# Kernel tuning notes

Hardware: AMD Instinct MI355X
Metric: run time of the kernel (lower is better)

## Reference

```python
import math
import jax, jax.numpy as jnp
import numpy as np

D_MODEL = 1024
NUM_HEADS = 16
MAX_SEQ_LEN = 2048
THETA = 10000.0


def setup_inputs() -> dict:
    key = jax.random.key(0)
    ks = jax.random.split(key, 5)
    B, S, D = 2, 2048, D_MODEL
    std = math.sqrt(2.0 / (D + D))
    x = jax.random.normal(ks[0], (B, S, D), dtype=jnp.float32)
    wq = jax.random.normal(ks[1], (D, D), dtype=jnp.float32) * std
    wk = jax.random.normal(ks[2], (D, D), dtype=jnp.float32) * std
    wv = jax.random.normal(ks[3], (D, D), dtype=jnp.float32) * std
    wo = jax.random.normal(ks[4], (D, D), dtype=jnp.float32) * std
    return {"x": x, "wq": wq, "wk": wk, "wv": wv, "wo": wo}


def _rope_tables(seq_len: int, d_k: int):
    # angles[i, k] = i / theta^(2k/d_k), k over d_k//2 pairs
    inv_freq = 1.0 / (THETA ** (jnp.arange(0, d_k, 2, dtype=jnp.float32) / d_k))
    angles = jnp.arange(seq_len, dtype=jnp.float32)[:, None] * inv_freq[None, :]  # [S, d_k/2]
    return jnp.cos(angles), jnp.sin(angles)


def _apply_rope(x, cos, sin):
    # x: [..., S, d_k]; cos/sin: [S, d_k/2], broadcast over leading dims
    x_even = x[..., ::2]
    x_odd = x[..., 1::2]
    r_even = x_even * cos - x_odd * sin
    r_odd = x_even * sin + x_odd * cos
    return jnp.stack([r_even, r_odd], axis=-1).reshape(x.shape)


def reference(x, wq, wk, wv, wo):
    B, S, D = x.shape
    H = NUM_HEADS
    dk = D // H

    def split_heads(t):  # [B,S,D] -> [B,H,S,dk]
        return t.reshape(B, S, H, dk).transpose(0, 2, 1, 3)

    Q = split_heads(x @ wq.T)
    K = split_heads(x @ wk.T)
    V = split_heads(x @ wv.T)

    cos, sin = _rope_tables(S, dk)
    Q = _apply_rope(Q, cos, sin)
    K = _apply_rope(K, cos, sin)

    scores = jnp.einsum('bhqd,bhkd->bhqk', Q, K) / jnp.sqrt(jnp.float32(dk))
    mask = jnp.tril(jnp.ones((S, S), dtype=bool))  # causal: q can attend k <= q
    neg_inf = jnp.float32(-jnp.inf)
    scores = jnp.where(mask, scores, neg_inf)
    m = jnp.max(scores, axis=-1, keepdims=True)
    m = jnp.where(jnp.isinf(m), jnp.zeros_like(m), m)
    exp_scores = jnp.exp(scores - m)
    exp_scores = jnp.where(mask, exp_scores, 0.0)
    attn = exp_scores / (jnp.sum(exp_scores, axis=-1, keepdims=True) + 1e-9)
    out = jnp.einsum('bhqk,bhkd->bhqd', attn, V)  # [B,H,S,dk]
    out = out.transpose(0, 2, 1, 3).reshape(B, S, D)
    return out @ wo.T
```

## Files before the change

### kernel.cpp

```cpp
#include <hip/hip_runtime.h>
#include <stdint.h>

typedef unsigned short u16;
typedef unsigned int u32;
typedef __bf16 bf16x8 __attribute__((ext_vector_type(8)));
typedef float f32x4 __attribute__((ext_vector_type(4)));
typedef unsigned short u16x8 __attribute__((ext_vector_type(8)));

#define D_MODEL 1024
#define SEQ 2048
#define NH 16
#define DK 64
#define NROWS 4096

static __device__ __forceinline__ u16 f2bf(float f) {
  u32 u = __float_as_uint(f);
  u = (u + 0x7FFFu + ((u >> 16) & 1u)) >> 16;
  return (u16)u;
}
static __device__ __forceinline__ float bf2f(u16 h) {
  return __uint_as_float(((u32)h) << 16);
}
static __device__ __forceinline__ f32x4 mfma16(bf16x8 a, bf16x8 b, f32x4 c) {
  return __builtin_amdgcn_mfma_f32_16x16x32_bf16(a, b, c, 0, 0, 0);
}
static __device__ __forceinline__ void gload16(const void* g, void* l) {
  __builtin_amdgcn_global_load_lds(
      (const __attribute__((address_space(1))) void*)g,
      (__attribute__((address_space(3))) void*)l, 16, 0, 0);
}

static __device__ __forceinline__ float xor32_max(float x) {
#if __has_builtin(__builtin_amdgcn_permlane32_swap)
  u32 a = __float_as_uint(x), b = a;
  auto pr = __builtin_amdgcn_permlane32_swap(a, b, false, false);
  return fmaxf(__uint_as_float(pr[0]), __uint_as_float(pr[1]));
#else
  return fmaxf(x, __shfl_xor(x, 32));
#endif
}
static __device__ __forceinline__ float xor32_add(float x) {
#if __has_builtin(__builtin_amdgcn_permlane32_swap)
  u32 a = __float_as_uint(x), b = a;
  auto pr = __builtin_amdgcn_permlane32_swap(a, b, false, false);
  return __uint_as_float(pr[0]) + __uint_as_float(pr[1]);
#else
  return x + __shfl_xor(x, 32);
#endif
}

__global__ __launch_bounds__(256) void k_cast(
    const float* __restrict__ x, const float* __restrict__ wq,
    const float* __restrict__ wk, const float* __restrict__ wv,
    const float* __restrict__ wo, u16* __restrict__ xb, u16* __restrict__ wqb,
    u16* __restrict__ wkb, u16* __restrict__ wvb, u16* __restrict__ wob,
    float* __restrict__ ct, float* __restrict__ st) {
  if (blockIdx.x >= 4096) {
    int i = (int)(blockIdx.x - 4096) * 256 + threadIdx.x;
    int s = i >> 5, p = i & 31;
    double ang = (double)s * pow(10000.0, -(double)p / 32.0);
    ct[i] = (float)cos(ang);
    st[i] = (float)sin(ang);
    return;
  }
  size_t e = ((size_t)blockIdx.x * 256 + threadIdx.x) * 8;
  const float* s;
  u16* d;
  size_t off;
  if (e < (size_t)NROWS * D_MODEL) {
    s = x; d = xb; off = e;
  } else {
    size_t r = e - (size_t)NROWS * D_MODEL;
    unsigned wi = (unsigned)(r >> 20);
    off = r & 1048575u;
    s = wi == 0 ? wq : wi == 1 ? wk : wi == 2 ? wv : wo;
    d = wi == 0 ? wqb : wi == 1 ? wkb : wi == 2 ? wvb : wob;
  }
  float4 a = *(const float4*)(s + off);
  float4 b = *(const float4*)(s + off + 4);
  u16x8 o;
  o[0] = f2bf(a.x); o[1] = f2bf(a.y); o[2] = f2bf(a.z); o[3] = f2bf(a.w);
  o[4] = f2bf(b.x); o[5] = f2bf(b.y); o[6] = f2bf(b.z); o[7] = f2bf(b.w);
  *(u16x8*)(d + off) = o;
}

__global__ __launch_bounds__(256, 1) void k_gemm3(
    const u16* __restrict__ A, const u16* __restrict__ B0,
    const u16* __restrict__ B1, const u16* __restrict__ B2,
    u16* __restrict__ Cb) {
  constexpr int K = 1024;
  const int mb = blockIdx.x, nb = blockIdx.y;
  const int tid = threadIdx.x;
  const int lane = tid & 63, w = tid >> 6;
  const int lq = lane & 15, lg = lane >> 4;
  const int wm = w >> 1, wn = w & 1;
  __shared__ __align__(16) u16 As[128 * 64];
  __shared__ __align__(16) u16 Bs[128 * 64];

  const int sel = nb >> 3;
  const u16* Bp = sel == 0 ? B0 : (sel == 1 ? B1 : B2);
  const int nloc = (nb & 7) * 128;
  const char* Ab = (const char*)A + (size_t)mb * 128 * 2048;
  const char* Bb = (const char*)Bp + (size_t)nloc * 2048;

  f32x4 zero4 = {0.f, 0.f, 0.f, 0.f};
  f32x4 acc[4][4];
#pragma unroll
  for (int i = 0; i < 4; ++i)
#pragma unroll
    for (int j = 0; j < 4; ++j) acc[i][j] = zero4;

  for (int k0 = 0; k0 < K; k0 += 64) {
#pragma unroll
    for (int c = 0; c < 4; ++c) {
      int ch = c * 256 + tid;
      int srow = ch >> 3;
      int scb = ((ch & 7) * 16) ^ ((srow & 7) << 4);
      const char* ga = Ab + (size_t)srow * 2048 + k0 * 2 + scb;
      const char* gb = Bb + (size_t)srow * 2048 + k0 * 2 + scb;
      gload16(ga, (char*)As + ch * 16);
      gload16(gb, (char*)Bs + ch * 16);
    }
    __syncthreads();
#pragma unroll
    for (int ks = 0; ks < 2; ++ks) {
      bf16x8 af[4], bfr[4];
#pragma unroll
      for (int i = 0; i < 4; ++i) {
        int ra = wm * 64 + i * 16 + lq;
        int rb = wn * 64 + i * 16 + lq;
        af[i] = *(const bf16x8*)((const char*)As +
                                 ra * 128 + ((ks * 64 + lg * 16) ^ ((ra & 7) << 4)));
        bfr[i] = *(const bf16x8*)((const char*)Bs +
                                  rb * 128 + ((ks * 64 + lg * 16) ^ ((rb & 7) << 4)));
      }
#pragma unroll
      for (int i = 0; i < 4; ++i)
#pragma unroll
        for (int j = 0; j < 4; ++j) acc[i][j] = mfma16(af[i], bfr[j], acc[i][j]);
    }
    __syncthreads();
  }

#pragma unroll
  for (int i = 0; i < 4; ++i) {
#pragma unroll
    for (int r = 0; r < 4; ++r) {
      size_t rowg = (size_t)(mb * 128 + wm * 64 + i * 16 + lg * 4 + r);
#pragma unroll
      for (int j = 0; j < 4; ++j) {
        int colg = nb * 128 + wn * 64 + j * 16 + lq;
        Cb[rowg * 3072 + colg] = f2bf(acc[i][j][r]);
      }
    }
  }
}

__global__ __launch_bounds__(256) void k_rope(const u16* __restrict__ qkv,
                                              const float* __restrict__ ct,
                                              const float* __restrict__ st,
                                              u16* __restrict__ qh, u16* __restrict__ kh) {
  int gi = blockIdx.x * 256 + threadIdx.x;
  int row = gi >> 7;
  int col = (gi & 127) << 3;
  int h = col >> 6, d0 = col & 63;
  int b = row >> 11, s = row & 2047;
  const int srcoff = blockIdx.y ? 1024 : 0;
  const float qs = blockIdx.y ? 1.0f : 0.18033688011112042f;
  u16x8 v = *(const u16x8*)(qkv + (size_t)row * 3072 + srcoff + col);
  const float* cp = ct + s * 32 + (d0 >> 1);
  const float* sp = st + s * 32 + (d0 >> 1);
  u16x8 o;
#pragma unroll
  for (int i = 0; i < 4; ++i) {
    float ev = bf2f(v[2 * i]), od = bf2f(v[2 * i + 1]);
    float c = cp[i], sn = sp[i];
    o[2 * i] = f2bf((ev * c - od * sn) * qs);
    o[2 * i + 1] = f2bf((ev * sn + od * c) * qs);
  }
  u16* dst = blockIdx.y ? kh : qh;
  *(u16x8*)(dst + (((size_t)(b * 16 + h) * SEQ + s) << 6) + d0) = o;
}

__global__ __launch_bounds__(256) void k_vtrans(const u16* __restrict__ qkv,
                                                u16* __restrict__ vt) {
  __shared__ __align__(16) u16 t[64][72];
  int sb = blockIdx.x, bh = blockIdx.y;
  int b = bh >> 4, h = bh & 15;
  int tid = threadIdx.x;
#pragma unroll
  for (int c = 0; c < 2; ++c) {
    int o = tid * 8 + c * 2048;
    int r = o >> 6, d = o & 63;
    u16x8 v = *(const u16x8*)(qkv + (size_t)(b * SEQ + sb * 64 + r) * 3072 + 2048 + h * 64 + d);
    *(u16x8*)&t[r][d] = v;
  }
  __syncthreads();
#pragma unroll
  for (int c = 0; c < 2; ++c) {
    int o = tid * 8 + c * 2048;
    int d = o >> 6, si = o & 63;
    u16x8 v;
#pragma unroll
    for (int j = 0; j < 8; ++j) v[j] = t[si + j][d];
    *(u16x8*)(vt + ((size_t)bh * 64 + d) * SEQ + sb * 64 + si) = v;
  }
}

__global__ __launch_bounds__(256, 2) void k_gemmo(const u16* __restrict__ A,
                                                  const u16* __restrict__ B0,
                                                  float* __restrict__ Cf) {
  constexpr int K = 1024;
  const int mb = blockIdx.x, nb = blockIdx.y;
  const int tid = threadIdx.x;
  const int lane = tid & 63, w = tid >> 6;
  const int lq = lane & 15, lg = lane >> 4;
  const int wm = w >> 1, wn = w & 1;
  __shared__ __align__(16) u16 As[128 * 64];
  __shared__ __align__(16) u16 Bs[64 * 64];

  const char* Ab = (const char*)A + (size_t)mb * 128 * 2048;
  const char* Bb = (const char*)B0 + (size_t)(nb * 64) * 2048;

  f32x4 zero4 = {0.f, 0.f, 0.f, 0.f};
  f32x4 acc[4][2];
#pragma unroll
  for (int i = 0; i < 4; ++i) {
    acc[i][0] = zero4; acc[i][1] = zero4;
  }

  for (int k0 = 0; k0 < K; k0 += 64) {
#pragma unroll
    for (int c = 0; c < 4; ++c) {
      int ch = c * 256 + tid;
      int srow = ch >> 3;
      int scb = ((ch & 7) * 16) ^ ((srow & 7) << 4);
      gload16(Ab + (size_t)srow * 2048 + k0 * 2 + scb, (char*)As + ch * 16);
      if (c < 2)
        gload16(Bb + (size_t)srow * 2048 + k0 * 2 + scb, (char*)Bs + ch * 16);
    }
    __syncthreads();
#pragma unroll
    for (int ks = 0; ks < 2; ++ks) {
      bf16x8 af[4], bfr[2];
#pragma unroll
      for (int i = 0; i < 4; ++i) {
        int ra = wm * 64 + i * 16 + lq;
        af[i] = *(const bf16x8*)((const char*)As +
                                 ra * 128 + ((ks * 64 + lg * 16) ^ ((ra & 7) << 4)));
      }
#pragma unroll
      for (int j = 0; j < 2; ++j) {
        int rb = wn * 32 + j * 16 + lq;
        bfr[j] = *(const bf16x8*)((const char*)Bs +
                                  rb * 128 + ((ks * 64 + lg * 16) ^ ((rb & 7) << 4)));
      }
#pragma unroll
      for (int i = 0; i < 4; ++i)
#pragma unroll
        for (int j = 0; j < 2; ++j) acc[i][j] = mfma16(af[i], bfr[j], acc[i][j]);
    }
    __syncthreads();
  }

#pragma unroll
  for (int i = 0; i < 4; ++i) {
#pragma unroll
    for (int r = 0; r < 4; ++r) {
      size_t rowg = (size_t)(mb * 128 + wm * 64 + i * 16 + lg * 4 + r);
#pragma unroll
      for (int j = 0; j < 2; ++j) {
        int colg = nb * 64 + wn * 32 + j * 16 + lq;
        Cf[rowg * 1024 + colg] = acc[i][j][r];
      }
    }
  }
}

static __device__ __forceinline__ void attn_tile(
    const u16* Kl, const u16* Vl, u16* Plw, int k0, int qrow, int lq, int lg,
    bf16x8 qf0, bf16x8 qf1, float& m_run, float& l_run, f32x4* accO, bool masked) {
  f32x4 zero4 = {0.f, 0.f, 0.f, 0.f};
  f32x4 sa[4];
  sa[0] = zero4; sa[1] = zero4; sa[2] = zero4; sa[3] = zero4;
  __builtin_amdgcn_s_setprio(1);
#pragma unroll
  for (int kt = 0; kt < 4; ++kt) {
    int krow = kt * 16 + lq;
    int base = krow * 128 + lg * 16;
    int swz = (krow & 7) << 4;
    bf16x8 kf0 = *(const bf16x8*)((const char*)Kl + (base ^ swz));
    bf16x8 kf1 = *(const bf16x8*)((const char*)Kl + ((base + 64) ^ swz));
    sa[kt] = mfma16(kf0, qf0, sa[kt]);
    sa[kt] = mfma16(kf1, qf1, sa[kt]);
  }
  __builtin_amdgcn_s_setprio(0);

  float p[16];
#pragma unroll
  for (int kt = 0; kt < 4; ++kt)
#pragma unroll
    for (int r = 0; r < 4; ++r) p[kt * 4 + r] = sa[kt][r];
  if (masked) {
#pragma unroll
    for (int kt = 0; kt < 4; ++kt)
#pragma unroll
      for (int r = 0; r < 4; ++r) {
        int key = k0 + kt * 16 + lg * 4 + r;
        if (key > qrow) p[kt * 4 + r] = -1e30f;
      }
  }
  float x0 = fmaxf(p[0], p[1]), x1 = fmaxf(p[2], p[3]);
  float x2 = fmaxf(p[4], p[5]), x3 = fmaxf(p[6], p[7]);
  float x4 = fmaxf(p[8], p[9]), x5 = fmaxf(p[10], p[11]);
  float x6 = fmaxf(p[12], p[13]), x7 = fmaxf(p[14], p[15]);
  x0 = fmaxf(x0, x1); x2 = fmaxf(x2, x3); x4 = fmaxf(x4, x5); x6 = fmaxf(x6, x7);
  x0 = fmaxf(x0, x2); x4 = fmaxf(x4, x6);
  float pm = fmaxf(x0, x4);
  pm = fmaxf(pm, __shfl_xor(pm, 16));
  pm = xor32_max(pm);
  const bool resc = __any(pm > m_run + 8.0f);
  float mnew = resc ? fmaxf(m_run, pm) : m_run;
#pragma unroll
  for (int i = 0; i < 16; ++i) p[i] = __builtin_amdgcn_exp2f(p[i] - mnew);
  float s0 = p[0] + p[1], s1 = p[2] + p[3], s2 = p[4] + p[5], s3 = p[6] + p[7];
  float s4 = p[8] + p[9], s5 = p[10] + p[11], s6 = p[12] + p[13], s7 = p[14] + p[15];
  s0 += s1; s2 += s3; s4 += s5; s6 += s7;
  s0 += s2; s4 += s6;
  float rs = s0 + s4;
  rs += __shfl_xor(rs, 16);
  rs = xor32_add(rs);
  if (resc) {
    float alpha = __builtin_amdgcn_exp2f(m_run - mnew);
    l_run = l_run * alpha + rs;
    m_run = mnew;
#pragma unroll
    for (int r = 0; r < 4; ++r) {
      float ar = __shfl(alpha, lg * 4 + r);
#pragma unroll
      for (int dt = 0; dt < 4; ++dt) accO[dt][r] *= ar;
    }
  } else {
    l_run += rs;
  }

  {
    int swz = (lq & 7) << 4;
#pragma unroll
    for (int kt = 0; kt < 4; ++kt) {
      u32 w0, w1;
      asm("v_cvt_pk_bf16_f32 %0, %1, %2"
          : "=v"(w0) : "v"(p[kt * 4 + 0]), "v"(p[kt * 4 + 1]));
      asm("v_cvt_pk_bf16_f32 %0, %1, %2"
          : "=v"(w1) : "v"(p[kt * 4 + 2]), "v"(p[kt * 4 + 3]));
      int a0 = (lq * 128 + (kt * 16 + lg * 4) * 2) ^ swz;
      int a1 = (lq * 128 + (kt * 16 + lg * 4 + 2) * 2) ^ swz;
      *(u32*)((char*)Plw + a0) = w0;
      *(u32*)((char*)Plw + a1) = w1;
    }
  }
  {
    int swz = (lq & 7) << 4;
    bf16x8 pa0 = *(const bf16x8*)((const char*)Plw + ((lq * 128 + lg * 16) ^ swz));
    bf16x8 pa1 = *(const bf16x8*)((const char*)Plw + ((lq * 128 + 64 + lg * 16) ^ swz));
    __builtin_amdgcn_s_setprio(1);
#pragma unroll
    for (int dt = 0; dt < 4; ++dt) {
      int vrow = dt * 16 + lq;
      int vb = vrow * 128 + lg * 16;
      int vs = (vrow & 7) << 4;
      bf16x8 v0 = *(const bf16x8*)((const char*)Vl + (vb ^ vs));
      bf16x8 v1 = *(const bf16x8*)((const char*)Vl + ((vb + 64) ^ vs));
      accO[dt] = mfma16(pa0, v0, accO[dt]);
      accO[dt] = mfma16(pa1, v1, accO[dt]);
    }
    __builtin_amdgcn_s_setprio(0);
  }
}

__global__ __launch_bounds__(256, 4) void k_attn(const u16* __restrict__ qh,
                                                 const u16* __restrict__ kh,
                                                 const u16* __restrict__ vt,
                                                 u16* __restrict__ ao) {
  const int qb1 = (int)blockIdx.x;
  const int qb2 = 31 - qb1;
  const int bh = blockIdx.y;
  const int tid = threadIdx.x;
  const int w = tid >> 6;
  const int lane = tid & 63;
  const int lq = lane & 15;
  const int lg = lane >> 4;

  __shared__ __align__(16) u16 Kd[2][64 * 64];
  __shared__ __align__(16) u16 Vd[2][64 * 64];
  __shared__ __align__(16) u16 Pl[4][16 * 64];

  const int qtop1 = qb1 * 64 + w * 16;
  const int qtop2 = qb2 * 64 + w * 16;
  const int qrow1 = qtop1 + lq;
  const int qrow2 = qtop2 + lq;

  const u16* qp1 = qh + ((size_t)bh * SEQ + qrow1) * DK + lg * 8;
  const u16* qp2 = qh + ((size_t)bh * SEQ + qrow2) * DK + lg * 8;
  bf16x8 qa0 = *(const bf16x8*)qp1;
  bf16x8 qa1 = *(const bf16x8*)(qp1 + 32);
  bf16x8 qc0 = *(const bf16x8*)qp2;
  bf16x8 qc1 = *(const bf16x8*)(qp2 + 32);

  f32x4 zero4 = {0.f, 0.f, 0.f, 0.f};
  f32x4 acc1[4], acc2[4];
#pragma unroll
  for (int dt = 0; dt < 4; ++dt) { acc1[dt] = zero4; acc2[dt] = zero4; }
  float m1 = -1e30f, l1 = 0.f, m2 = -1e30f, l2 = 0.f;

  const int nt1 = qb1 + 1;
  const int NT = qb2 + 1;

  const char* kb_ = (const char*)kh + (size_t)bh * SEQ * 128;
  const char* vb_ = (const char*)vt + (size_t)bh * DK * 4096;

#pragma unroll
  for (int pass = 0; pass < 2; ++pass) {
    int chunk = pass * 256 + tid;
    int srow = chunk >> 3;
    int colb = ((chunk & 7) * 16) ^ ((srow & 7) << 4);
    gload16(kb_ + (size_t)srow * 128 + colb, (char*)Kd[0] + chunk * 16);
    gload16(vb_ + (size_t)srow * 4096 + colb, (char*)Vd[0] + chunk * 16);
  }
  __syncthreads();

  for (int t = 0; t < NT; ++t) {
    const int cur = t & 1;
    if (t + 1 < NT) {
      int kb0 = (t + 1) * 64;
#pragma unroll
      for (int pass = 0; pass < 2; ++pass) {
        int chunk = pass * 256 + tid;
        int srow = chunk >> 3;
        int colb = ((chunk & 7) * 16) ^ ((srow & 7) << 4);
        gload16(kb_ + (size_t)(kb0 + srow) * 128 + colb,
                (char*)Kd[cur ^ 1] + chunk * 16);
        gload16(vb_ + (size_t)srow * 4096 + kb0 * 2 + colb,
                (char*)Vd[cur ^ 1] + chunk * 16);
      }
    }
    const int k0 = t * 64;
    if (t < nt1)
      attn_tile(Kd[cur], Vd[cur], Pl[w], k0, qrow1, lq, lg, qa0, qa1,
                m1, l1, acc1, t == nt1 - 1);
    attn_tile(Kd[cur], Vd[cur], Pl[w], k0, qrow2, lq, lg, qc0, qc1,
              m2, l2, acc2, t == NT - 1);
    __syncthreads();
  }

  const int b = bh >> 4, h = bh & 15;
#pragma unroll
  for (int r = 0; r < 4; ++r) {
    float lr = __shfl(l1, lg * 4 + r);
    float inv = 1.f / (lr + 1e-9f);
    int qq = qtop1 + lg * 4 + r;
    u16* orow = ao + ((size_t)b * SEQ + qq) * D_MODEL + h * DK;
#pragma unroll
    for (int dt = 0; dt < 4; ++dt) orow[dt * 16 + lq] = f2bf(acc1[dt][r] * inv);
  }
#pragma unroll
  for (int r = 0; r < 4; ++r) {
    float lr = __shfl(l2, lg * 4 + r);
    float inv = 1.f / (lr + 1e-9f);
    int qq = qtop2 + lg * 4 + r;
    u16* orow = ao + ((size_t)b * SEQ + qq) * D_MODEL + h * DK;
#pragma unroll
    for (int dt = 0; dt < 4; ++dt) orow[dt * 16 + lq] = f2bf(acc2[dt][r] * inv);
  }
}

extern "C" void kernel_launch(void* const* d_in, const int* in_sizes, int n_in,
                              void* d_out, int out_size, void* d_ws, size_t ws_size,
                              hipStream_t stream) {
  const float* x = (const float*)d_in[0];
  const float* wq = (const float*)d_in[1];
  const float* wk = (const float*)d_in[2];
  const float* wv = (const float*)d_in[3];
  const float* wo = (const float*)d_in[4];
  float* out = (float*)d_out;
  char* ws = (char*)d_ws;

  u16* xb   = (u16*)(ws + 0);
  u16* wqb  = (u16*)(ws + 8388608);
  u16* wkb  = (u16*)(ws + 10485760);
  u16* wvb  = (u16*)(ws + 12582912);
  u16* wob  = (u16*)(ws + 14680064);
  u16* qkv  = (u16*)(ws + 16777216);
  u16* qhb  = (u16*)(ws + 41943040);
  u16* khb  = (u16*)(ws + 50331648);
  u16* vtb  = (u16*)(ws + 58720256);
  u16* aob  = (u16*)(ws + 67108864);
  float* ct = (float*)(ws + 75497472);
  float* st = (float*)(ws + 75759616);

  k_cast<<<4352, 256, 0, stream>>>(x, wq, wk, wv, wo, xb, wqb, wkb, wvb, wob, ct, st);
  k_gemm3<<<dim3(32, 24), 256, 0, stream>>>(xb, wqb, wkb, wvb, qkv);
  k_rope<<<dim3(2048, 2), 256, 0, stream>>>(qkv, ct, st, qhb, khb);
  k_vtrans<<<dim3(32, 32), 256, 0, stream>>>(qkv, vtb);
  k_attn<<<dim3(16, 32), 256, 0, stream>>>(qhb, khb, vtb, aob);
  k_gemmo<<<dim3(32, 16), 256, 0, stream>>>(aob, wob, out);
}
```

Baseline: 113.9 us.

## Split paired causal query blocks into separate attention blocks with balanced ordering

Each attention block used to handle two query tiles, qb and 31-qb, to balance the causal work. The kernel now handles one query tile per block over a 1024-block grid. The block index is remapped so that light and heavy query tiles are interleaved across four dispatch waves. The aim is more parallelism and occupancy, at the cost of loading each K/V tile twice instead of sharing it between two query tiles.

```diff
diff --git a/kernel.cpp b/kernel.cpp
--- a/kernel.cpp
+++ b/kernel.cpp
@@ -382,9 +382,12 @@
                                                  const u16* __restrict__ kh,
                                                  const u16* __restrict__ vt,
                                                  u16* __restrict__ ao) {
-  const int qb1 = (int)blockIdx.x;
-  const int qb2 = 31 - qb1;
-  const int bh = blockIdx.y;
+  const int id = (int)blockIdx.x;
+  const int g = id & 255;
+  const int s_ = id >> 8;
+  const int bh = g >> 3;
+  const int j = g & 7;
+  const int qb = s_ == 0 ? j : (s_ == 1 ? 15 - j : (s_ == 2 ? 16 + j : 31 - j));
   const int tid = threadIdx.x;
   const int w = tid >> 6;
   const int lane = tid & 63;
@@ -395,26 +398,20 @@
   __shared__ __align__(16) u16 Vd[2][64 * 64];
   __shared__ __align__(16) u16 Pl[4][16 * 64];
 
-  const int qtop1 = qb1 * 64 + w * 16;
-  const int qtop2 = qb2 * 64 + w * 16;
-  const int qrow1 = qtop1 + lq;
-  const int qrow2 = qtop2 + lq;
-
-  const u16* qp1 = qh + ((size_t)bh * SEQ + qrow1) * DK + lg * 8;
-  const u16* qp2 = qh + ((size_t)bh * SEQ + qrow2) * DK + lg * 8;
-  bf16x8 qa0 = *(const bf16x8*)qp1;
-  bf16x8 qa1 = *(const bf16x8*)(qp1 + 32);
-  bf16x8 qc0 = *(const bf16x8*)qp2;
-  bf16x8 qc1 = *(const bf16x8*)(qp2 + 32);
+  const int qtop = qb * 64 + w * 16;
+  const int qrow = qtop + lq;
+
+  const u16* qp = qh + ((size_t)bh * SEQ + qrow) * DK + lg * 8;
+  bf16x8 qf0 = *(const bf16x8*)qp;
+  bf16x8 qf1 = *(const bf16x8*)(qp + 32);
 
   f32x4 zero4 = {0.f, 0.f, 0.f, 0.f};
-  f32x4 acc1[4], acc2[4];
-#pragma unroll
-  for (int dt = 0; dt < 4; ++dt) { acc1[dt] = zero4; acc2[dt] = zero4; }
-  float m1 = -1e30f, l1 = 0.f, m2 = -1e30f, l2 = 0.f;
-
-  const int nt1 = qb1 + 1;
-  const int NT = qb2 + 1;
+  f32x4 acc[4];
+#pragma unroll
+  for (int dt = 0; dt < 4; ++dt) acc[dt] = zero4;
+  float m_run = -1e30f, l_run = 0.f;
+
+  const int NT = qb + 1;
 
   const char* kb_ = (const char*)kh + (size_t)bh * SEQ * 128;
   const char* vb_ = (const char*)vt + (size_t)bh * DK * 4096;
@@ -444,33 +441,20 @@
                 (char*)Vd[cur ^ 1] + chunk * 16);
       }
     }
-    const int k0 = t * 64;
-    if (t < nt1)
-      attn_tile(Kd[cur], Vd[cur], Pl[w], k0, qrow1, lq, lg, qa0, qa1,
-                m1, l1, acc1, t == nt1 - 1);
-    attn_tile(Kd[cur], Vd[cur], Pl[w], k0, qrow2, lq, lg, qc0, qc1,
-              m2, l2, acc2, t == NT - 1);
+    attn_tile(Kd[cur], Vd[cur], Pl[w], t * 64, qrow, lq, lg, qf0, qf1,
+              m_run, l_run, acc, t == NT - 1);
     __syncthreads();
   }
 
   const int b = bh >> 4, h = bh & 15;
 #pragma unroll
   for (int r = 0; r < 4; ++r) {
-    float lr = __shfl(l1, lg * 4 + r);
+    float lr = __shfl(l_run, lg * 4 + r);
     float inv = 1.f / (lr + 1e-9f);
-    int qq = qtop1 + lg * 4 + r;
+    int qq = qtop + lg * 4 + r;
     u16* orow = ao + ((size_t)b * SEQ + qq) * D_MODEL + h * DK;
 #pragma unroll
-    for (int dt = 0; dt < 4; ++dt) orow[dt * 16 + lq] = f2bf(acc1[dt][r] * inv);
-  }
-#pragma unroll
-  for (int r = 0; r < 4; ++r) {
-    float lr = __shfl(l2, lg * 4 + r);
-    float inv = 1.f / (lr + 1e-9f);
-    int qq = qtop2 + lg * 4 + r;
-    u16* orow = ao + ((size_t)b * SEQ + qq) * D_MODEL + h * DK;
-#pragma unroll
-    for (int dt = 0; dt < 4; ++dt) orow[dt * 16 + lq] = f2bf(acc2[dt][r] * inv);
+    for (int dt = 0; dt < 4; ++dt) orow[dt * 16 + lq] = f2bf(acc[dt][r] * inv);
   }
 }
 
@@ -502,6 +486,6 @@
   k_gemm3<<<dim3(32, 24), 256, 0, stream>>>(xb, wqb, wkb, wvb, qkv);
   k_rope<<<dim3(2048, 2), 256, 0, stream>>>(qkv, ct, st, qhb, khb);
   k_vtrans<<<dim3(32, 32), 256, 0, stream>>>(qkv, vtb);
-  k_attn<<<dim3(16, 32), 256, 0, stream>>>(qhb, khb, vtb, aob);
+  k_attn<<<1024, 256, 0, stream>>>(qhb, khb, vtb, aob);
   k_gemmo<<<dim3(32, 16), 256, 0, stream>>>(aob, wob, out);
 }
```

Result: no change. 113.2 us (-0.7%).
